# Kernel optimization log

Measured on AMD Instinct MI355X. Metric: run time of the kernel, lower is better.

Reference implementation:

```python
import jax, jax.numpy as jnp
import numpy as np

B, T, D = 2, 2048, 1024
H = 16
HD = D // H


def setup_inputs() -> dict:
    key = jax.random.key(0)
    ks = jax.random.split(key, 9)
    s = 1.0 / np.sqrt(D)
    return {
        "x": jax.random.normal(ks[0], (B, T, D), dtype=jnp.float32),
        "Wq": jax.random.normal(ks[1], (D, D), dtype=jnp.float32) * s,
        "bq": jax.random.normal(ks[2], (D,), dtype=jnp.float32) * s,
        "Wk": jax.random.normal(ks[3], (D, D), dtype=jnp.float32) * s,
        "bk": jax.random.normal(ks[4], (D,), dtype=jnp.float32) * s,
        "Wv": jax.random.normal(ks[5], (D, D), dtype=jnp.float32) * s,
        "bv": jax.random.normal(ks[6], (D,), dtype=jnp.float32) * s,
        "Wo": jax.random.normal(ks[7], (D, D), dtype=jnp.float32) * s,
        "bo": jax.random.normal(ks[8], (D,), dtype=jnp.float32) * s,
    }


def reference(x, Wq, bq, Wk, bk, Wv, bv, Wo, bo):
    b, t, d = x.shape
    # projections; torch Linear computes x @ W.T + b
    def proj(W, bias):
        y = jnp.einsum("btd,ed->bte", x, W) + bias
        return y.reshape(b, t, H, HD).transpose(0, 2, 1, 3)  # [B,H,T,HD]
    q = proj(Wq, bq)
    k = proj(Wk, bk)
    v = proj(Wv, bv)
    scores = jnp.einsum("bhqd,bhkd->bhqk", q, k) / np.sqrt(HD)  # [B,H,T,T]
    causal = jnp.triu(jnp.ones((t, t), dtype=bool), k=1)
    scores = jnp.where(causal[None, None], jnp.float32(-1e9), scores)
    attn = jax.nn.softmax(scores, axis=-1)
    out = jnp.einsum("bhqk,bhkd->bhqd", attn, v)  # [B,H,T,HD]
    out = out.transpose(0, 2, 1, 3).reshape(b, t, d)
    return jnp.einsum("btd,ed->bte", out, Wo) + bo
```

## Files before the change

### kernel.cpp

```cpp
#include <hip/hip_runtime.h>


#define DEV __device__ __forceinline__

typedef __attribute__((ext_vector_type(8))) __bf16 bf16x8;
typedef __attribute__((ext_vector_type(4))) float f32x4;

DEV unsigned short f2bf(float f) {
  union { float f; unsigned u; } c;
  c.f = f;
  unsigned u = c.u + 0x7FFFu + ((c.u >> 16) & 1u);
  return (unsigned short)(u >> 16);
}

DEV unsigned cvtpk(float lo, float hi) {
  unsigned r;
  asm("v_cvt_pk_bf16_f32 %0, %1, %2" : "=v"(r) : "v"(lo), "v"(hi));
  return r;
}

DEV void gload16(const unsigned short* g, unsigned short* l) {
  __builtin_amdgcn_global_load_lds(
      (const __attribute__((address_space(1))) unsigned int*)g,
      (__attribute__((address_space(3))) unsigned int*)l, 16, 0, 0);
}

DEV f32x4 mfma16(bf16x8 a, bf16x8 b, f32x4 c) {
  return __builtin_amdgcn_mfma_f32_16x16x32_bf16(a, b, c, 0, 0, 0);
}

#define WAITVM(n) asm volatile("s_waitcnt vmcnt(" #n ")" ::: "memory")
#define WAITLGKM() asm volatile("s_waitcnt lgkmcnt(0)" ::: "memory")
#define BAR() __builtin_amdgcn_s_barrier()
#define SCHEDB() __builtin_amdgcn_sched_barrier(0)
#define PRIO(n) __builtin_amdgcn_s_setprio(n)

__global__ __launch_bounds__(256) void k_cvt_all(
    const float* __restrict__ x, const float* __restrict__ wq,
    const float* __restrict__ wk, const float* __restrict__ wv,
    const float* __restrict__ wo, unsigned short* __restrict__ dst) {
  int i = blockIdx.x * blockDim.x + threadIdx.x;
  const float* s;
  int off;
  if (i < 1048576) {
    s = x; off = i;
  } else {
    int j = i - 1048576;
    int w = j >> 18;
    off = j & 262143;
    s = (w == 0) ? wq : (w == 1) ? wk : (w == 2) ? wv : wo;
  }
  float4 v = reinterpret_cast<const float4*>(s)[off];
  uint2 o;
  o.x = (unsigned)f2bf(v.x) | ((unsigned)f2bf(v.y) << 16);
  o.y = (unsigned)f2bf(v.z) | ((unsigned)f2bf(v.w) << 16);
  reinterpret_cast<uint2*>(dst)[i] = o;
}

DEV void gemm_stage(const unsigned short* __restrict__ A,
                    const unsigned short* __restrict__ W,
                    unsigned short* la, unsigned short* lb,
                    int m0, int n0, int k0, int tid) {
#pragma unroll
  for (int i = 0; i < 2; ++i) {
    const int c = i * 256 + tid;
    const int row = c >> 2;
    const int scb = (((c & 3) << 4)) ^ ((row & 3) << 4);
    gload16(A + (m0 + row) * 1024 + k0 + (scb >> 1),
            (unsigned short*)((char*)la + c * 16));
    gload16(W + (n0 + row) * 1024 + k0 + (scb >> 1),
            (unsigned short*)((char*)lb + c * 16));
  }
}

DEV void gemm_core_128(const unsigned short* __restrict__ A,
                       const unsigned short* __restrict__ W,
                       unsigned short* la0, unsigned short* lb0,
                       int m0, int n0, f32x4 (&acc)[4][4]) {
  const int tid = threadIdx.x;
  const int lane = tid & 63;
  const int wave = tid >> 6;
  const int wm = (wave >> 1) * 64, wn = (wave & 1) * 64;
  const int g16 = ((lane >> 4) << 4);
  const int sx = (lane & 3) << 4;

  gemm_stage(A, W, la0, lb0, m0, n0, 0, tid);
  __syncthreads();

  for (int kt = 0; kt < 32; ++kt) {
    const int cur = kt & 1;
    unsigned short* la = la0 + cur * 4096;
    unsigned short* lb = lb0 + cur * 4096;
    if (kt + 1 < 32)
      gemm_stage(A, W, la0 + (cur ^ 1) * 4096, lb0 + (cur ^ 1) * 4096, m0, n0,
                 (kt + 1) * 32, tid);
    bf16x8 af[4], bfr[4];
#pragma unroll
    for (int m = 0; m < 4; ++m)
      af[m] = *reinterpret_cast<const bf16x8*>(
          (char*)la + (wm + m * 16 + (lane & 15)) * 64 + (g16 ^ sx));
#pragma unroll
    for (int n = 0; n < 4; ++n)
      bfr[n] = *reinterpret_cast<const bf16x8*>(
          (char*)lb + (wn + n * 16 + (lane & 15)) * 64 + (g16 ^ sx));
#pragma unroll
    for (int m = 0; m < 4; ++m)
#pragma unroll
      for (int n = 0; n < 4; ++n)
        acc[m][n] = mfma16(af[m], bfr[n], acc[m][n]);
    __syncthreads();
  }
}

__global__ __launch_bounds__(256) void k_gemm_qkv(
    const unsigned short* __restrict__ X, const unsigned short* __restrict__ Wq,
    const unsigned short* __restrict__ Wk, const unsigned short* __restrict__ Wv,
    const float* __restrict__ bq, const float* __restrict__ bk,
    const float* __restrict__ bv, unsigned short* __restrict__ Qo,
    unsigned short* __restrict__ Ko, unsigned short* __restrict__ Vo) {
  __shared__ unsigned short ls[16384];
  const int id = blockIdx.x;
  const int xcd = id & 7, s4 = id >> 3;
  const int mode = s4 >> 5;
  const int bx = ((s4 >> 3) & 3) * 2 + (xcd & 1);
  const int by = (s4 & 7) * 4 + (xcd >> 1);
  const unsigned short* W = (mode == 0) ? Wq : (mode == 1) ? Wk : Wv;
  const float* bias = (mode == 0) ? bq : (mode == 1) ? bk : bv;
  const int m0 = by * 128, n0 = bx * 128;
  f32x4 acc[4][4] = {};
  gemm_core_128(X, W, ls, ls + 8192, m0, n0, acc);

  const int lane = threadIdx.x & 63, wave = threadIdx.x >> 6;
  const int l15 = lane & 15, g = lane >> 4;
  const int wm = (wave >> 1) * 64, wn = (wave & 1) * 64;
  unsigned short* lw = ls + wave * 4096;

  const int h = (n0 + wn) >> 6;
  const int rbase0 = m0 + wm;
  const int b = rbase0 >> 11;
  const int tb0 = rbase0 & 2047;

  if (mode == 2) {
#pragma unroll
    for (int m = 0; m < 4; ++m)
#pragma unroll
      for (int n = 0; n < 4; ++n) {
        const float bb = bias[n0 + wn + n * 16 + l15];
        uint2 w;
        w.x = cvtpk(acc[m][n][0] + bb, acc[m][n][1] + bb);
        w.y = cvtpk(acc[m][n][2] + bb, acc[m][n][3] + bb);
        *reinterpret_cast<uint2*>(
            (char*)lw + (n * 16 + l15) * 128 +
            ((((m << 2) + g) ^ (l15 & 14)) << 3)) = w;
      }
    WAITLGKM();
    SCHEDB();
#pragma unroll
    for (int it = 0; it < 8; ++it) {
      const int hd = (lane >> 3) + it * 8;
      const int jj = ((lane & 7) << 1) ^ (hd & 14);
      uint4 v = *reinterpret_cast<const uint4*>((char*)lw + hd * 128 + jj * 8);
      *reinterpret_cast<uint4*>(
          &Vo[((((b << 4) + h) << 6) + hd) * 2048 + tb0 + ((lane & 7) << 3)]) =
          v;
    }
  } else {
    const float sc = (mode == 0) ? 0.180336880f : 1.0f;
#pragma unroll
    for (int m = 0; m < 4; ++m)
#pragma unroll
      for (int n = 0; n < 4; ++n) {
        const float bb = bias[n0 + wn + n * 16 + l15];
#pragma unroll
        for (int r = 0; r < 4; ++r)
          lw[(m * 16 + (g << 2) + r) * 64 + n * 16 + l15] =
              f2bf((acc[m][n][r] + bb) * sc);
      }
    WAITLGKM();
    SCHEDB();
    unsigned short* dst = (mode == 0) ? Qo : Ko;
#pragma unroll
    for (int it = 0; it < 8; ++it) {
      const int rr = (lane >> 3) + it * 8;
      const int ck = (lane & 7) * 8;
      uint4 v = *reinterpret_cast<const uint4*>(&lw[rr * 64 + ck]);
      *reinterpret_cast<uint4*>(
          &dst[(((b << 4) + h) * 2048 + tb0 + rr) * 64 + ck]) = v;
    }
  }
}

__global__ __launch_bounds__(256) void k_gemm_out(
    const unsigned short* __restrict__ Ctx, const unsigned short* __restrict__ Wo,
    const float* __restrict__ bo, float* __restrict__ Out) {
  __shared__ unsigned short ls[16384];
  unsigned short* la0 = ls;
  unsigned short* lb0 = ls + 8192;
  const int id = blockIdx.x;
  const int xcd = id & 7, s4 = id >> 3;
  const int bx = ((s4 >> 3) & 7) * 2 + (xcd & 1);
  const int by = (s4 & 7) * 4 + (xcd >> 1);
  const int tid = threadIdx.x;
  const int lane = tid & 63, wave = tid >> 6;
  const int l15 = lane & 15, g = lane >> 4;
  const int m0 = by * 128, n0 = bx * 64;
  const int wm = (wave >> 1) * 64, wn = (wave & 1) * 32;
  const int g16 = (g << 4);
  const int sx = (lane & 3) << 4;
  f32x4 acc[4][2] = {};

#define STG_OUT(buf, k0)                                                     \
  {                                                                          \
    _Pragma("unroll") for (int i = 0; i < 2; ++i) {                          \
      const int c = i * 256 + tid;                                           \
      const int row = c >> 2;                                                \
      const int scb = (((c & 3) << 4)) ^ ((row & 3) << 4);                   \
      gload16(Ctx + (m0 + row) * 1024 + (k0) + (scb >> 1),                   \
              (unsigned short*)((char*)(la0 + (buf)*4096) + c * 16));        \
    }                                                                        \
    {                                                                        \
      const int row = tid >> 2;                                              \
      const int scb = (((tid & 3) << 4)) ^ ((row & 3) << 4);                 \
      gload16(Wo + (n0 + row) * 1024 + (k0) + (scb >> 1),                    \
              (unsigned short*)((char*)(lb0 + (buf)*2048) + tid * 16));      \
    }                                                                        \
  }

  STG_OUT(0, 0);
  __syncthreads();

  for (int kt = 0; kt < 32; ++kt) {
    const int cur = kt & 1;
    unsigned short* la = la0 + cur * 4096;
    unsigned short* lb = lb0 + cur * 2048;
    if (kt + 1 < 32) STG_OUT(cur ^ 1, (kt + 1) * 32);
    bf16x8 af[4], bfr[2];
#pragma unroll
    for (int m = 0; m < 4; ++m)
      af[m] = *reinterpret_cast<const bf16x8*>(
          (char*)la + (wm + m * 16 + l15) * 64 + (g16 ^ sx));
#pragma unroll
    for (int n = 0; n < 2; ++n)
      bfr[n] = *reinterpret_cast<const bf16x8*>(
          (char*)lb + (wn + n * 16 + l15) * 64 + (g16 ^ sx));
#pragma unroll
    for (int m = 0; m < 4; ++m)
#pragma unroll
      for (int n = 0; n < 2; ++n)
        acc[m][n] = mfma16(af[m], bfr[n], acc[m][n]);
    __syncthreads();
  }
#undef STG_OUT

  float* lwf = (float*)(ls + wave * 4096);
#pragma unroll
  for (int m = 0; m < 4; ++m)
#pragma unroll
    for (int n = 0; n < 2; ++n) {
      const float bb = bo[n0 + wn + n * 16 + l15];
#pragma unroll
      for (int r = 0; r < 4; ++r)
        lwf[(m * 16 + (g << 2) + r) * 32 + n * 16 + l15] = acc[m][n][r] + bb;
    }
  WAITLGKM();
  SCHEDB();
#pragma unroll
  for (int it = 0; it < 8; ++it) {
    const int rr = (lane >> 3) + it * 8;
    const int ck = (lane & 7) * 4;
    float4 v = *reinterpret_cast<const float4*>(&lwf[rr * 32 + ck]);
    *reinterpret_cast<float4*>(&Out[(m0 + wm + rr) * 1024 + n0 + wn + ck]) = v;
  }
}


DEV void attn_stage128(const unsigned short* __restrict__ Kb,
                       const unsigned short* __restrict__ Vb,
                       unsigned short* lk, unsigned short* lv, int kv0,
                       int tid) {
#pragma unroll
  for (int i = 0; i < 2; ++i) {
    const int c = i * 512 + tid;
    const int krow = c >> 3;
    const int kscb = ((c & 7) << 4) ^ ((krow & 7) << 4);
    gload16(Kb + (kv0 + krow) * 64 + (kscb >> 1),
            (unsigned short*)((char*)lk + c * 16));
    const int vrow = c >> 4;
    const int vscb = ((c & 15) << 4) ^ ((vrow & 7) << 4);
    gload16(Vb + vrow * 2048 + kv0 + (vscb >> 1),
            (unsigned short*)((char*)lv + c * 16));
  }
}

DEV void attn_step(const unsigned short* lk128, int s,
                   const unsigned short* lv128,
                   unsigned short (&lp)[16][64], const bf16x8 (&qf)[2],
                   f32x4 (&o)[4], float& lsum, int lane, int qloc, bool diag) {
  const int g = lane >> 4;
  const int l15 = lane & 15;
  f32x4 st[4];
  PRIO(1);
#pragma unroll
  for (int n = 0; n < 4; ++n) {
    f32x4 z = {};
    const int row = n * 16 + l15;
    const int sw = (row & 7) << 4;
#pragma unroll
    for (int kk = 0; kk < 2; ++kk) {
      bf16x8 kf = *reinterpret_cast<const bf16x8*>(
          (char*)lk128 + (s * 64 + row) * 128 + ((kk * 64 + (g << 4)) ^ sw));
      z = mfma16(kf, qf[kk], z);
    }
    st[n] = z;
  }
  PRIO(0);
  if (diag) {
#pragma unroll
    for (int n = 0; n < 4; ++n)
#pragma unroll
      for (int r = 0; r < 4; ++r)
        if (n * 16 + g * 4 + r > qloc) st[n][r] = -1e30f;
  }
  float rs = 0.f;
#pragma unroll
  for (int n = 0; n < 4; ++n)
#pragma unroll
    for (int r = 0; r < 4; ++r) {
      float p = exp2f(st[n][r]);
      st[n][r] = p;
      rs += p;
    }
  lsum += rs;
  const int psw = (l15 & 7) << 4;
#pragma unroll
  for (int n = 0; n < 4; ++n) {
    uint2 w;
    w.x = cvtpk(st[n][0], st[n][1]);
    w.y = cvtpk(st[n][2], st[n][3]);
    *reinterpret_cast<uint2*>(
        (char*)lp + l15 * 128 + (((n << 5) | (g << 3)) ^ psw)) = w;
  }
  WAITLGKM();
  SCHEDB();
  bf16x8 pb[2];
  pb[0] = *reinterpret_cast<const bf16x8*>(
      (char*)lp + l15 * 128 + (((g << 4)) ^ psw));
  pb[1] = *reinterpret_cast<const bf16x8*>(
      (char*)lp + l15 * 128 + ((64 + (g << 4)) ^ psw));
  PRIO(1);
#pragma unroll
  for (int h = 0; h < 4; ++h) {
    const int vr = h * 16 + l15;
    const int sw = (vr & 7) << 4;
#pragma unroll
    for (int kk = 0; kk < 2; ++kk) {
      bf16x8 vf = *reinterpret_cast<const bf16x8*>(
          (char*)lv128 + vr * 256 + ((s * 128 + kk * 64 + (g << 4)) ^ sw));
      o[h] = mfma16(vf, pb[kk], o[h]);
    }
  }
  PRIO(0);
}

DEV void attn_epi(unsigned short* __restrict__ Ctx,
                  unsigned short (&lp)[16][64], const f32x4 (&o)[4],
                  float lsum, int b, int hh, int qbase, int lane) {
  float lt = lsum;
  lt += __shfl_xor(lt, 16);
  lt += __shfl_xor(lt, 32);
  const float inv = 1.f / lt;
  const int g = lane >> 4;
  const int l15 = lane & 15;
  const int psw = (l15 & 7) << 4;
#pragma unroll
  for (int h = 0; h < 4; ++h) {
    uint2 w;
    w.x = cvtpk(o[h][0] * inv, o[h][1] * inv);
    w.y = cvtpk(o[h][2] * inv, o[h][3] * inv);
    *reinterpret_cast<uint2*>(
        (char*)lp + l15 * 128 + (((h << 5) | (g << 3)) ^ psw)) = w;
  }
  WAITLGKM();
  SCHEDB();
#pragma unroll
  for (int it = 0; it < 2; ++it) {
    const int q = (lane >> 3) + it * 8;
    const int blk = (lane & 7) ^ (q & 7);
    uint4 v = *reinterpret_cast<const uint4*>((char*)lp + q * 128 + blk * 16);
    *reinterpret_cast<uint4*>(
        &Ctx[(b * 2048 + qbase + q) * 1024 + hh * 64 + ((lane & 7) << 3)]) = v;
  }
}

__global__ __launch_bounds__(512) void k_attn(
    const unsigned short* __restrict__ Q, const unsigned short* __restrict__ K,
    const unsigned short* __restrict__ Vt, unsigned short* __restrict__ Ctx) {
  __shared__ unsigned short lk[2][8192];
  __shared__ unsigned short lv[2][8192];
  __shared__ unsigned short lp[8][16][64];

  const int tid = threadIdx.x, lane = tid & 63, wave = tid >> 6;
  const int id = blockIdx.x;
  const int xcd = id & 7, r4 = id >> 3;
  const int ip = r4 & 15;
  const int bh = ((r4 >> 4) << 3) + xcd;

  const int qtA = ip;
  const int qtB = 31 - ip;
  const int nb = (qtB >> 1) + 1;

  const bool isB = wave < 4;
  const int wv4 = wave & 3;
  const int qt = isB ? qtB : qtA;

  const unsigned short* Kb = K + bh * 2048 * 64;
  const unsigned short* Vb = Vt + bh * 64 * 2048;

  bf16x8 qf[2];
  {
    const unsigned short* qr =
        Q + (bh * 2048 + qt * 64 + wv4 * 16 + (lane & 15)) * 64 +
        ((lane >> 4) << 3);
    qf[0] = *reinterpret_cast<const bf16x8*>(qr);
    qf[1] = *reinterpret_cast<const bf16x8*>(qr + 32);
  }

  f32x4 o[4] = {};
  float lsum = 0.f;
  const int qloc = wv4 * 16 + (lane & 15);

  attn_stage128(Kb, Vb, lk[0], lv[0], 0, tid);

  for (int t = 0; t < nb; ++t) {
    WAITVM(0);
    BAR();
    {
      const int nx = (t + 1 < nb) ? t + 1 : nb - 1;
      attn_stage128(Kb, Vb, lk[(t + 1) & 1], lv[(t + 1) & 1], nx * 128, tid);
    }
    SCHEDB();
    const unsigned short* lkc = lk[t & 1];
    const unsigned short* lvc = lv[t & 1];
#pragma unroll
    for (int s = 0; s < 2; ++s) {
      const int sub = 2 * t + s;
      if (sub <= qt)
        attn_step(lkc, s, lvc, lp[wave], qf, o, lsum, lane, qloc, sub == qt);
    }
  }

  WAITVM(0);

  const int b = bh >> 4, hh = bh & 15;
  attn_epi(Ctx, lp[wave], o, lsum, b, hh, qt * 64 + wv4 * 16, lane);
}

extern "C" void kernel_launch(void* const* d_in, const int* in_sizes, int n_in,
                              void* d_out, int out_size, void* d_ws,
                              size_t ws_size, hipStream_t stream) {
  const float* x = (const float*)d_in[0];
  const float* Wq = (const float*)d_in[1];
  const float* bq = (const float*)d_in[2];
  const float* Wk = (const float*)d_in[3];
  const float* bk = (const float*)d_in[4];
  const float* Wv = (const float*)d_in[5];
  const float* bv = (const float*)d_in[6];
  const float* Wo = (const float*)d_in[7];
  const float* bo = (const float*)d_in[8];
  float* out = (float*)d_out;

  char* ws = (char*)d_ws;
  unsigned short* xb = (unsigned short*)(ws);
  unsigned short* wqb = (unsigned short*)(ws + (8u << 20));
  unsigned short* wkb = (unsigned short*)(ws + (10u << 20));
  unsigned short* wvb = (unsigned short*)(ws + (12u << 20));
  unsigned short* wob = (unsigned short*)(ws + (14u << 20));
  unsigned short* Qb = (unsigned short*)(ws + (16u << 20));
  unsigned short* Kb = (unsigned short*)(ws + (24u << 20));
  unsigned short* Vtb = (unsigned short*)(ws + (32u << 20));
  unsigned short* Ctx = (unsigned short*)(ws + (40u << 20));

  k_cvt_all<<<8192, 256, 0, stream>>>(x, Wq, Wk, Wv, Wo, xb);

  k_gemm_qkv<<<768, 256, 0, stream>>>(xb, wqb, wkb, wvb, bq, bk, bv,
                                      Qb, Kb, Vtb);
  k_attn<<<512, 512, 0, stream>>>(Qb, Kb, Vtb, Ctx);
  k_gemm_out<<<512, 256, 0, stream>>>(Ctx, wob, bo, out);
}
```

Baseline: 110.7 us.

## Fuse Q/K/V projections into one block sharing the X tile

The QKV GEMM now computes all three projections per block: each block loads one 128x32 X tile and three 64-row weight tiles, and keeps three accumulator sets. This lets the three projections share each X tile load from global memory and LDS, where before each projection reloaded it, and the grid shrinks from 768 to 512 blocks. In exchange it uses more LDS and registers per block (three accumulators), and the tile is narrower (128x64 per weight), which may lower occupancy and MFMA efficiency per B fragment.

```diff
diff --git a/kernel.cpp b/kernel.cpp
--- a/kernel.cpp
+++ b/kernel.cpp
@@ -57,136 +57,164 @@
   reinterpret_cast<uint2*>(dst)[i] = o;
 }
 
-DEV void gemm_stage(const unsigned short* __restrict__ A,
-                    const unsigned short* __restrict__ W,
-                    unsigned short* la, unsigned short* lb,
-                    int m0, int n0, int k0, int tid) {
-#pragma unroll
-  for (int i = 0; i < 2; ++i) {
-    const int c = i * 256 + tid;
-    const int row = c >> 2;
-    const int scb = (((c & 3) << 4)) ^ ((row & 3) << 4);
-    gload16(A + (m0 + row) * 1024 + k0 + (scb >> 1),
-            (unsigned short*)((char*)la + c * 16));
-    gload16(W + (n0 + row) * 1024 + k0 + (scb >> 1),
-            (unsigned short*)((char*)lb + c * 16));
-  }
-}
-
-DEV void gemm_core_128(const unsigned short* __restrict__ A,
-                       const unsigned short* __restrict__ W,
-                       unsigned short* la0, unsigned short* lb0,
-                       int m0, int n0, f32x4 (&acc)[4][4]) {
-  const int tid = threadIdx.x;
-  const int lane = tid & 63;
-  const int wave = tid >> 6;
-  const int wm = (wave >> 1) * 64, wn = (wave & 1) * 64;
-  const int g16 = ((lane >> 4) << 4);
-  const int sx = (lane & 3) << 4;
-
-  gemm_stage(A, W, la0, lb0, m0, n0, 0, tid);
-  __syncthreads();
-
-  for (int kt = 0; kt < 32; ++kt) {
-    const int cur = kt & 1;
-    unsigned short* la = la0 + cur * 4096;
-    unsigned short* lb = lb0 + cur * 4096;
-    if (kt + 1 < 32)
-      gemm_stage(A, W, la0 + (cur ^ 1) * 4096, lb0 + (cur ^ 1) * 4096, m0, n0,
-                 (kt + 1) * 32, tid);
-    bf16x8 af[4], bfr[4];
-#pragma unroll
-    for (int m = 0; m < 4; ++m)
-      af[m] = *reinterpret_cast<const bf16x8*>(
-          (char*)la + (wm + m * 16 + (lane & 15)) * 64 + (g16 ^ sx));
-#pragma unroll
-    for (int n = 0; n < 4; ++n)
-      bfr[n] = *reinterpret_cast<const bf16x8*>(
-          (char*)lb + (wn + n * 16 + (lane & 15)) * 64 + (g16 ^ sx));
-#pragma unroll
-    for (int m = 0; m < 4; ++m)
-#pragma unroll
-      for (int n = 0; n < 4; ++n)
-        acc[m][n] = mfma16(af[m], bfr[n], acc[m][n]);
-    __syncthreads();
-  }
-}
-
 __global__ __launch_bounds__(256) void k_gemm_qkv(
     const unsigned short* __restrict__ X, const unsigned short* __restrict__ Wq,
     const unsigned short* __restrict__ Wk, const unsigned short* __restrict__ Wv,
     const float* __restrict__ bq, const float* __restrict__ bk,
     const float* __restrict__ bv, unsigned short* __restrict__ Qo,
     unsigned short* __restrict__ Ko, unsigned short* __restrict__ Vo) {
-  __shared__ unsigned short ls[16384];
+  __shared__ unsigned short ls[20480];
+  unsigned short* la0 = ls;
+  unsigned short* lbq = ls + 8192;
+  unsigned short* lbk = ls + 12288;
+  unsigned short* lbv = ls + 16384;
+
   const int id = blockIdx.x;
   const int xcd = id & 7, s4 = id >> 3;
-  const int mode = s4 >> 5;
-  const int bx = ((s4 >> 3) & 3) * 2 + (xcd & 1);
+  const int bx = ((s4 >> 3) & 7) * 2 + (xcd & 1);
   const int by = (s4 & 7) * 4 + (xcd >> 1);
-  const unsigned short* W = (mode == 0) ? Wq : (mode == 1) ? Wk : Wv;
-  const float* bias = (mode == 0) ? bq : (mode == 1) ? bk : bv;
-  const int m0 = by * 128, n0 = bx * 128;
-  f32x4 acc[4][4] = {};
-  gemm_core_128(X, W, ls, ls + 8192, m0, n0, acc);
-
-  const int lane = threadIdx.x & 63, wave = threadIdx.x >> 6;
+  const int m0 = by * 128, n0 = bx * 64;
+
+  const int tid = threadIdx.x;
+  const int lane = tid & 63, wave = tid >> 6;
   const int l15 = lane & 15, g = lane >> 4;
-  const int wm = (wave >> 1) * 64, wn = (wave & 1) * 64;
-  unsigned short* lw = ls + wave * 4096;
-
+  const int wm = (wave >> 1) * 64, wn = (wave & 1) * 32;
+  const int g16 = g << 4;
+  const int sx = (lane & 3) << 4;
+
+  f32x4 a0[4][2] = {}, a1[4][2] = {}, a2[4][2] = {};
+
+#define STG_QKV(buf, k0)                                                     \
+  {                                                                          \
+    _Pragma("unroll") for (int i = 0; i < 2; ++i) {                          \
+      const int c = i * 256 + tid;                                           \
+      const int row = c >> 2;                                                \
+      const int scb = ((c & 3) << 4) ^ ((row & 3) << 4);                     \
+      gload16(X + (m0 + row) * 1024 + (k0) + (scb >> 1),                     \
+              (unsigned short*)((char*)(la0 + (buf)*4096) + c * 16));        \
+    }                                                                        \
+    {                                                                        \
+      const int row = tid >> 2;                                              \
+      const int scb = ((tid & 3) << 4) ^ ((row & 3) << 4);                   \
+      const int go = (n0 + row) * 1024 + (k0) + (scb >> 1);                  \
+      gload16(Wq + go,                                                       \
+              (unsigned short*)((char*)(lbq + (buf)*2048) + tid * 16));      \
+      gload16(Wk + go,                                                       \
+              (unsigned short*)((char*)(lbk + (buf)*2048) + tid * 16));      \
+      gload16(Wv + go,                                                       \
+              (unsigned short*)((char*)(lbv + (buf)*2048) + tid * 16));      \
+    }                                                                        \
+  }
+
+  STG_QKV(0, 0);
+  __syncthreads();
+
+  for (int kt = 0; kt < 32; ++kt) {
+    const int cur = kt & 1;
+    if (kt + 1 < 32) STG_QKV(cur ^ 1, (kt + 1) * 32);
+    unsigned short* la = la0 + cur * 4096;
+    bf16x8 af[4];
+#pragma unroll
+    for (int m = 0; m < 4; ++m)
+      af[m] = *reinterpret_cast<const bf16x8*>(
+          (char*)la + (wm + m * 16 + l15) * 64 + (g16 ^ sx));
+    {
+      unsigned short* lb = lbq + cur * 2048;
+      bf16x8 bfr[2];
+#pragma unroll
+      for (int n = 0; n < 2; ++n)
+        bfr[n] = *reinterpret_cast<const bf16x8*>(
+            (char*)lb + (wn + n * 16 + l15) * 64 + (g16 ^ sx));
+#pragma unroll
+      for (int m = 0; m < 4; ++m)
+#pragma unroll
+        for (int n = 0; n < 2; ++n) a0[m][n] = mfma16(af[m], bfr[n], a0[m][n]);
+    }
+    {
+      unsigned short* lb = lbk + cur * 2048;
+      bf16x8 bfr[2];
+#pragma unroll
+      for (int n = 0; n < 2; ++n)
+        bfr[n] = *reinterpret_cast<const bf16x8*>(
+            (char*)lb + (wn + n * 16 + l15) * 64 + (g16 ^ sx));
+#pragma unroll
+      for (int m = 0; m < 4; ++m)
+#pragma unroll
+        for (int n = 0; n < 2; ++n) a1[m][n] = mfma16(af[m], bfr[n], a1[m][n]);
+    }
+    {
+      unsigned short* lb = lbv + cur * 2048;
+      bf16x8 bfr[2];
+#pragma unroll
+      for (int n = 0; n < 2; ++n)
+        bfr[n] = *reinterpret_cast<const bf16x8*>(
+            (char*)lb + (wn + n * 16 + l15) * 64 + (g16 ^ sx));
+#pragma unroll
+      for (int m = 0; m < 4; ++m)
+#pragma unroll
+        for (int n = 0; n < 2; ++n) a2[m][n] = mfma16(af[m], bfr[n], a2[m][n]);
+    }
+    __syncthreads();
+  }
+#undef STG_QKV
+
+  unsigned short* lw = ls + wave * 2048;
   const int h = (n0 + wn) >> 6;
-  const int rbase0 = m0 + wm;
-  const int b = rbase0 >> 11;
-  const int tb0 = rbase0 & 2047;
-
-  if (mode == 2) {
+  const int hd0 = (n0 + wn) & 63;
+  const int rb = m0 + wm;
+  const int b = rb >> 11;
+  const int tb0 = rb & 2047;
+
+#pragma unroll
+  for (int mode = 0; mode < 2; ++mode) {
+    const float* bias = mode ? bk : bq;
+    const float sc = mode ? 1.0f : 0.180336880f;
+    unsigned short* dst = mode ? Ko : Qo;
+    WAITLGKM();
 #pragma unroll
     for (int m = 0; m < 4; ++m)
 #pragma unroll
-      for (int n = 0; n < 4; ++n) {
+      for (int n = 0; n < 2; ++n) {
         const float bb = bias[n0 + wn + n * 16 + l15];
-        uint2 w;
-        w.x = cvtpk(acc[m][n][0] + bb, acc[m][n][1] + bb);
-        w.y = cvtpk(acc[m][n][2] + bb, acc[m][n][3] + bb);
-        *reinterpret_cast<uint2*>(
-            (char*)lw + (n * 16 + l15) * 128 +
-            ((((m << 2) + g) ^ (l15 & 14)) << 3)) = w;
+        const f32x4 av = mode ? a1[m][n] : a0[m][n];
+#pragma unroll
+        for (int r = 0; r < 4; ++r)
+          lw[(m * 16 + (g << 2) + r) * 32 + n * 16 + l15] =
+              f2bf((av[r] + bb) * sc);
       }
     WAITLGKM();
     SCHEDB();
 #pragma unroll
-    for (int it = 0; it < 8; ++it) {
-      const int hd = (lane >> 3) + it * 8;
-      const int jj = ((lane & 7) << 1) ^ (hd & 14);
-      uint4 v = *reinterpret_cast<const uint4*>((char*)lw + hd * 128 + jj * 8);
+    for (int it = 0; it < 4; ++it) {
+      const int rr = (lane >> 2) + it * 16;
+      const int ck = (lane & 3) * 8;
+      uint4 v = *reinterpret_cast<const uint4*>(&lw[rr * 32 + ck]);
       *reinterpret_cast<uint4*>(
-          &Vo[((((b << 4) + h) << 6) + hd) * 2048 + tb0 + ((lane & 7) << 3)]) =
-          v;
-    }
-  } else {
-    const float sc = (mode == 0) ? 0.180336880f : 1.0f;
-#pragma unroll
-    for (int m = 0; m < 4; ++m)
-#pragma unroll
-      for (int n = 0; n < 4; ++n) {
-        const float bb = bias[n0 + wn + n * 16 + l15];
-#pragma unroll
-        for (int r = 0; r < 4; ++r)
-          lw[(m * 16 + (g << 2) + r) * 64 + n * 16 + l15] =
-              f2bf((acc[m][n][r] + bb) * sc);
-      }
-    WAITLGKM();
-    SCHEDB();
-    unsigned short* dst = (mode == 0) ? Qo : Ko;
-#pragma unroll
-    for (int it = 0; it < 8; ++it) {
-      const int rr = (lane >> 3) + it * 8;
-      const int ck = (lane & 7) * 8;
-      uint4 v = *reinterpret_cast<const uint4*>(&lw[rr * 64 + ck]);
-      *reinterpret_cast<uint4*>(
-          &dst[(((b << 4) + h) * 2048 + tb0 + rr) * 64 + ck]) = v;
-    }
+          &dst[(((b << 4) + h) * 2048 + tb0 + rr) * 64 + hd0 + ck]) = v;
+    }
+  }
+
+  WAITLGKM();
+#pragma unroll
+  for (int m = 0; m < 4; ++m)
+#pragma unroll
+    for (int n = 0; n < 2; ++n) {
+      const float bb = bv[n0 + wn + n * 16 + l15];
+      uint2 w;
+      w.x = cvtpk(a2[m][n][0] + bb, a2[m][n][1] + bb);
+      w.y = cvtpk(a2[m][n][2] + bb, a2[m][n][3] + bb);
+      *reinterpret_cast<uint2*>(&lw[(n * 16 + l15) * 64 + m * 16 + (g << 2)]) =
+          w;
+    }
+  WAITLGKM();
+  SCHEDB();
+#pragma unroll
+  for (int it = 0; it < 4; ++it) {
+    const int hdr = (lane >> 3) + it * 8;
+    const int ck = (lane & 7) * 8;
+    uint4 v = *reinterpret_cast<const uint4*>(&lw[hdr * 64 + ck]);
+    *reinterpret_cast<uint4*>(
+        &Vo[(((b << 4) + h) * 64 + hd0 + hdr) * 2048 + tb0 + ck]) = v;
   }
 }
 
@@ -482,7 +510,7 @@
 
   k_cvt_all<<<8192, 256, 0, stream>>>(x, Wq, Wk, Wv, Wo, xb);
 
-  k_gemm_qkv<<<768, 256, 0, stream>>>(xb, wqb, wkb, wvb, bq, bk, bv,
+  k_gemm_qkv<<<512, 256, 0, stream>>>(xb, wqb, wkb, wvb, bq, bk, bv,
                                       Qb, Kb, Vtb);
   k_attn<<<512, 512, 0, stream>>>(Qb, Kb, Vtb, Ctx);
   k_gemm_out<<<512, 256, 0, stream>>>(Ctx, wob, bo, out);
```

After: 106.8 us. 3.5% less time.
